# Kernel tuning notes

Hardware: AMD Instinct MI355X
Metric: run time of the kernel (lower is better)

## Reference

```python
import jax, jax.numpy as jnp
import numpy as np

EPS = 1e-5

def _layernorm(x, g, b):
    mu = jnp.mean(x, axis=-1, keepdims=True)
    var = jnp.var(x, axis=-1, keepdims=True)
    return (x - mu) * jax.lax.rsqrt(var + EPS) * g + b

def _pos_encoding(S, D, dtype):
    pos = jnp.arange(S, dtype=jnp.float32)[:, None]
    div = jnp.exp(jnp.arange(0, D, 2, dtype=jnp.float32) * (-jnp.log(10000.0) / D))
    pe = jnp.zeros((S, D), dtype=jnp.float32)
    pe = pe.at[:, 0::2].set(jnp.sin(pos * div))
    pe = pe.at[:, 1::2].set(jnp.cos(pos * div))
    return pe.astype(dtype)

def setup_inputs() -> dict:
    key = jax.random.key(0)
    B, S, D, H, F, L = 4, 1024, 768, 12, 3072, 6
    ks = jax.random.split(key, 8)
    s = 0.02
    return {
        "x": jax.random.normal(ks[0], (B, S, D), jnp.float32),
        "Wqkv": jax.random.normal(ks[1], (L, D, 3 * D), jnp.float32) * s,
        "bqkv": jnp.zeros((L, 3 * D), jnp.float32),
        "Wo": jax.random.normal(ks[2], (L, D, D), jnp.float32) * s,
        "bo": jnp.zeros((L, D), jnp.float32),
        "ln1_g": jnp.ones((L, D), jnp.float32),
        "ln1_b": jnp.zeros((L, D), jnp.float32),
        "W1": jax.random.normal(ks[3], (L, D, F), jnp.float32) * s,
        "b1": jnp.zeros((L, F), jnp.float32),
        "W2": jax.random.normal(ks[4], (L, F, D), jnp.float32) * s,
        "b2": jnp.zeros((L, D), jnp.float32),
        "ln2_g": jnp.ones((L, D), jnp.float32),
        "ln2_b": jnp.zeros((L, D), jnp.float32),
        "lnf_g": jnp.ones((D,), jnp.float32),
        "lnf_b": jnp.zeros((D,), jnp.float32),
        "num_heads": 12,
    }

def reference(x, Wqkv, bqkv, Wo, bo, ln1_g, ln1_b, W1, b1, W2, b2, ln2_g, ln2_b, lnf_g, lnf_b, num_heads):
    B, S, D = x.shape
    H = num_heads
    hd = D // H
    scale = 1.0 / jnp.sqrt(jnp.float32(hd)).astype(x.dtype)

    x = x + _pos_encoding(S, D, x.dtype)[None]

    def layer(h, params):
        wqkv, bq, wo, bo_, g1, b1_, w1, bias1, w2, bias2, g2, b2_ = params
        qkv = (h @ wqkv + bq).reshape(B, S, 3, H, hd)
        q, k, v = jnp.moveaxis(qkv, 2, 0)          # each [B,S,H,hd]
        q = q.transpose(0, 2, 1, 3)                 # bhqd
        k = k.transpose(0, 2, 1, 3)
        v = v.transpose(0, 2, 1, 3)
        scores = jnp.einsum('bhqd,bhkd->bhqk', q, k) * scale
        w = jax.nn.softmax(scores, axis=-1)
        w = jnp.clip(w, 1e-6, 1.0)                  # clamp as in torch module
        attn = jnp.einsum('bhqk,bhkd->bhqd', w, v)
        attn = attn.transpose(0, 2, 1, 3).reshape(B, S, D) @ wo + bo_
        h = _layernorm(h + attn, g1, b1_)
        ffn = jax.nn.relu(h @ w1 + bias1) @ w2 + bias2
        h = _layernorm(h + ffn, g2, b2_)
        return h, None

    params = (Wqkv, bqkv, Wo, bo, ln1_g, ln1_b, W1, b1, W2, b2, ln2_g, ln2_b)
    x, _ = jax.lax.scan(layer, x, params)
    return _layernorm(x, lnf_g, lnf_b)
```

## Files before the change

kernel.cpp:

```cpp
#include <hip/hip_runtime.h>
#include <math.h>

typedef float f32x4 __attribute__((ext_vector_type(4)));
typedef __bf16 bf16x8 __attribute__((ext_vector_type(8)));
typedef unsigned short u16x8 __attribute__((ext_vector_type(8)));

__device__ __forceinline__ unsigned short f2bf(float f) {
    union { float f; unsigned int u; } v; v.f = f;
    unsigned int r = v.u + 0x7FFFu + ((v.u >> 16) & 1u);
    return (unsigned short)(r >> 16);
}
__device__ __forceinline__ unsigned short f2bft(float f) {
    union { float f; unsigned int u; } v; v.f = f;
    return (unsigned short)(v.u >> 16);
}
__device__ __forceinline__ float bf2f(unsigned short u) {
    union { unsigned int u; float f; } v; v.u = ((unsigned int)u) << 16;
    return v.f;
}
__device__ __forceinline__ bf16x8 ld8(const unsigned short* p) {
    union { u16x8 u; bf16x8 b; } c;
    c.u = *(const u16x8*)p;
    return c.b;
}
__device__ __forceinline__ void gload_lds16(const unsigned short* g, unsigned short* l) {
    __builtin_amdgcn_global_load_lds(
        (const __attribute__((address_space(1))) unsigned int*)g,
        (__attribute__((address_space(3))) unsigned int*)l,
        16, 0, 0);
}
__device__ __forceinline__ int swz_off(int row, int quad) {
    return row * 32 + ((quad ^ ((row >> 1) & 3)) << 3);
}

__global__ __launch_bounds__(256)
void wprep_k(const float* __restrict__ Wqkv, const float* __restrict__ Wo,
             const float* __restrict__ W1, const float* __restrict__ W2,
             unsigned short* __restrict__ qkvT, unsigned short* __restrict__ woT,
             unsigned short* __restrict__ w1T, unsigned short* __restrict__ w2T) {
    __shared__ float tile[32][33];
    int bid = blockIdx.x;
    size_t ly = blockIdx.y;
    const float* W; unsigned short* Wt; int K, N, idx;
    if (bid < 1728)      { W = Wqkv + ly * 768 * 2304; Wt = qkvT + ly * 768 * 2304; K = 768;  N = 2304; idx = bid; }
    else if (bid < 2304) { W = Wo   + ly * 768 * 768;  Wt = woT  + ly * 768 * 768;  K = 768;  N = 768;  idx = bid - 1728; }
    else if (bid < 4608) { W = W1   + ly * 768 * 3072; Wt = w1T  + ly * 768 * 3072; K = 768;  N = 3072; idx = bid - 2304; }
    else                 { W = W2   + ly * 3072 * 768; Wt = w2T  + ly * 3072 * 768; K = 3072; N = 768;  idx = bid - 4608; }
    int ntile = N / 32;
    int n0 = (idx % ntile) * 32, k0 = (idx / ntile) * 32;
    int tx = threadIdx.x & 31, ty = threadIdx.x >> 5;
#pragma unroll
    for (int i = 0; i < 4; ++i) {
        int k = ty + i * 8;
        tile[k][tx] = W[(size_t)(k0 + k) * N + n0 + tx];
    }
    __syncthreads();
#pragma unroll
    for (int i = 0; i < 4; ++i) {
        int n = ty + i * 8;
        Wt[(size_t)(n0 + n) * K + k0 + tx] = f2bf(tile[tx][n]);
    }
}

__global__ __launch_bounds__(256)
void posenc_k(const float* __restrict__ x, float* __restrict__ h,
              unsigned short* __restrict__ hb) {
    int idx = blockIdx.x * 256 + threadIdx.x;
    const int TOT = 4 * 1024 * 768;
    if (idx >= TOT) return;
    int d = idx % 768;
    int s = (idx / 768) % 1024;
    int i2 = d >> 1;
    float dv = expf(-(float)(2 * i2) * (9.210340371976184f / 768.0f));
    float ang = (float)s * dv;
    float pe = (d & 1) ? cosf(ang) : sinf(ang);
    float v = x[idx] + pe;
    h[idx] = v;
    hb[idx] = f2bf(v);
}

template<int RELU, int BIAS, int QSCALE>
__global__ __launch_bounds__(256)
void gemm_k(const unsigned short* __restrict__ A, const unsigned short* __restrict__ Bt,
            const float* __restrict__ bias, unsigned short* __restrict__ Cb,
            int M, int N, int K, int Kc) {
    __shared__ unsigned short As[2][128 * 32];
    __shared__ unsigned short Bs[2][128 * 32];
    const int tid = threadIdx.x;
    const int lane = tid & 63, wave = tid >> 6;
    const int l15 = lane & 15, quad = lane >> 4;
    const int m0 = blockIdx.y * 128, n0 = blockIdx.x * 128;
    const int wr = (wave >> 1) * 64, wc = (wave & 1) * 64;
    const int kstart = blockIdx.z * Kc;
    unsigned short* Cbp = Cb + (size_t)blockIdx.z * M * N;

    const int r0 = wave * 32 + (lane >> 2);
    const int kc0 = lane & 3;

    auto stage = [&](int k0, int bi) {
#pragma unroll
        for (int j = 0; j < 2; ++j) {
            int r = r0 + j * 16;
            int kcl = kc0 ^ ((r >> 1) & 3);
            gload_lds16(A + (size_t)(m0 + r) * K + k0 + kcl * 8,
                        &As[bi][(wave * 32 + j * 16) * 32]);
            gload_lds16(Bt + (size_t)(n0 + r) * K + k0 + kcl * 8,
                        &Bs[bi][(wave * 32 + j * 16) * 32]);
        }
    };

    f32x4 acc[4][4];
#pragma unroll
    for (int i = 0; i < 4; ++i)
#pragma unroll
        for (int j = 0; j < 4; ++j) acc[i][j] = (f32x4){0.f, 0.f, 0.f, 0.f};

    stage(kstart, 0);
    const int nk = Kc / 32;
    for (int t = 0; t < nk; ++t) {
        __syncthreads();
        if (t + 1 < nk) stage(kstart + (t + 1) * 32, (t + 1) & 1);
        const unsigned short* Asb = As[t & 1];
        const unsigned short* Bsb = Bs[t & 1];
        bf16x8 af[4], bfr[4];
#pragma unroll
        for (int mt = 0; mt < 4; ++mt)
            af[mt] = ld8(&Asb[swz_off(wr + mt * 16 + l15, quad)]);
#pragma unroll
        for (int nt = 0; nt < 4; ++nt)
            bfr[nt] = ld8(&Bsb[swz_off(wc + nt * 16 + l15, quad)]);
#pragma unroll
        for (int mt = 0; mt < 4; ++mt)
#pragma unroll
            for (int nt = 0; nt < 4; ++nt)
                acc[mt][nt] = __builtin_amdgcn_mfma_f32_16x16x32_bf16(
                    af[mt], bfr[nt], acc[mt][nt], 0, 0, 0);
    }
    const float scl = (QSCALE && n0 < 768) ? 0.18033688088889765f : 1.0f;
#pragma unroll
    for (int mt = 0; mt < 4; ++mt)
#pragma unroll
        for (int nt = 0; nt < 4; ++nt)
#pragma unroll
            for (int r = 0; r < 4; ++r) {
                int row = m0 + wr + mt * 16 + quad * 4 + r;
                int col = n0 + wc + nt * 16 + l15;
                float v = acc[mt][nt][r];
                if (BIAS) v += bias[col];
                if (QSCALE) v *= scl;
                if (RELU) v = fmaxf(v, 0.f);
                Cbp[(size_t)row * N + col] = f2bf(v);
            }
}

__global__ __launch_bounds__(256)
void vt_prep(const unsigned short* __restrict__ qkv, unsigned short* __restrict__ Vt) {
    __shared__ unsigned short t[64][65];
    int bh = blockIdx.y, s0 = blockIdx.x * 64;
    int b = bh / 12, h = bh % 12;
    int tid = threadIdx.x;
    int tx = tid & 63, ty = tid >> 6;
#pragma unroll
    for (int r = 0; r < 16; ++r) {
        int i = ty + r * 4;
        t[i][tx] = qkv[(size_t)(b * 1024 + s0 + i) * 2304 + 1536 + h * 64 + tx];
    }
    __syncthreads();
#pragma unroll
    for (int r = 0; r < 16; ++r) {
        int dd = ty + r * 4;
        Vt[((size_t)bh * 64 + dd) * 1024 + s0 + tx] = t[tx][dd];
    }
}

__global__ __launch_bounds__(256)
void flash_k(const unsigned short* __restrict__ QKV, const unsigned short* __restrict__ Vt,
             unsigned short* __restrict__ O2, float* __restrict__ ls) {
    const int S = 1024, HD = 64;
    int bh = blockIdx.y, b = bh / 12, h = bh % 12;
    int q0 = blockIdx.x * 64;
    int zz = blockIdx.z;
    const unsigned short* Qp = QKV + (size_t)(b * 1024 + q0) * 2304 + h * 64;
    const unsigned short* Kp = QKV + (size_t)(b * 1024) * 2304 + 768 + h * 64;
    const unsigned short* Vp = Vt + (size_t)bh * HD * S;

    __shared__ unsigned short sm[20480];
    unsigned short* Qs = sm;

    int tid = threadIdx.x, lane = tid & 63, wave = tid >> 6;
    int l15 = lane & 15, quad = lane >> 4;
    const int rl0 = lane >> 2, c0 = lane & 3;

#pragma unroll
    for (int j = 0; j < 2; ++j) {
        int R = wave * 32 + j * 16 + rl0;
        int khalf = R >> 6, grow = R & 63;
        int lch = c0 ^ ((R >> 1) & 3);
        gload_lds16(Qp + (size_t)grow * 2304 + khalf * 32 + lch * 8,
                    &Qs[(wave * 32 + j * 16) * 32]);
    }
    __syncthreads();
    bf16x8 qa0 = ld8(&Qs[swz_off(wave * 16 + l15, quad)]);
    bf16x8 qa1 = ld8(&Qs[swz_off(64 + wave * 16 + l15, quad)]);

    auto stageKV = [&](int kt, int bi) {
        unsigned short* Ksb = sm + 4096 + bi * 4096;
        unsigned short* Vsb = sm + 12288 + bi * 4096;
#pragma unroll
        for (int j = 0; j < 2; ++j) {
            int R = wave * 32 + j * 16 + rl0;
            int khalf = R >> 6, grow = R & 63;
            int lch = c0 ^ ((R >> 1) & 3);
            gload_lds16(Kp + (size_t)(kt * 64 + grow) * 2304 + khalf * 32 + lch * 8,
                        &Ksb[(wave * 32 + j * 16) * 32]);
            gload_lds16(Vp + (size_t)grow * S + kt * 64 + khalf * 32 + lch * 8,
                        &Vsb[(wave * 32 + j * 16) * 32]);
        }
    };

    f32x4 o[4];
#pragma unroll
    for (int i = 0; i < 4; ++i) o[i] = (f32x4){0.f, 0.f, 0.f, 0.f};
    f32x4 lacc = (f32x4){0.f, 0.f, 0.f, 0.f};
    bf16x8 ones;
    {
        union { u16x8 u; bf16x8 b; } c;
#pragma unroll
        for (int j = 0; j < 8; ++j) c.u[j] = 0x3F80;
        ones = c.b;
    }
    unsigned short* Pw = sm + wave * 1024;

    stageKV(zz * 8, 0);
    for (int i = 0; i < 8; ++i) {
        int kt = zz * 8 + i;
        __syncthreads();
        if (i < 7) stageKV(kt + 1, (i + 1) & 1);
        const unsigned short* Ks = sm + 4096 + (i & 1) * 4096;
        const unsigned short* Vs = sm + 12288 + (i & 1) * 4096;

        f32x4 sc[4];
#pragma unroll
        for (int cb = 0; cb < 4; ++cb) {
            bf16x8 kb0 = ld8(&Ks[swz_off(cb * 16 + l15, quad)]);
            bf16x8 kb1 = ld8(&Ks[swz_off(64 + cb * 16 + l15, quad)]);
            f32x4 z = (f32x4){0.f, 0.f, 0.f, 0.f};
            z = __builtin_amdgcn_mfma_f32_16x16x32_bf16(qa0, kb0, z, 0, 0, 0);
            z = __builtin_amdgcn_mfma_f32_16x16x32_bf16(qa1, kb1, z, 0, 0, 0);
            sc[cb] = z;
        }
#pragma unroll
        for (int cb = 0; cb < 4; ++cb)
#pragma unroll
            for (int r = 0; r < 4; ++r)
                Pw[(quad * 4 + r) * 64 + ((cb * 16 + l15) ^ (quad << 4))] =
                    f2bft(__builtin_amdgcn_exp2f(sc[cb][r]));
        bf16x8 pa0 = ld8(&Pw[l15 * 64 + ((quad * 8) ^ ((l15 >> 2) << 4))]);
        bf16x8 pa1 = ld8(&Pw[l15 * 64 + ((32 + quad * 8) ^ ((l15 >> 2) << 4))]);
        lacc = __builtin_amdgcn_mfma_f32_16x16x32_bf16(pa0, ones, lacc, 0, 0, 0);
        lacc = __builtin_amdgcn_mfma_f32_16x16x32_bf16(pa1, ones, lacc, 0, 0, 0);
#pragma unroll
        for (int cb = 0; cb < 4; ++cb) {
            bf16x8 vb0 = ld8(&Vs[swz_off(cb * 16 + l15, quad)]);
            bf16x8 vb1 = ld8(&Vs[swz_off(64 + cb * 16 + l15, quad)]);
            o[cb] = __builtin_amdgcn_mfma_f32_16x16x32_bf16(pa0, vb0, o[cb], 0, 0, 0);
            o[cb] = __builtin_amdgcn_mfma_f32_16x16x32_bf16(pa1, vb1, o[cb], 0, 0, 0);
        }
    }
    unsigned short* Op = O2 + (size_t)zz * 4096 * 768;
#pragma unroll
    for (int cb = 0; cb < 4; ++cb)
#pragma unroll
        for (int r = 0; r < 4; ++r) {
            int row = q0 + wave * 16 + quad * 4 + r;
            Op[((size_t)(b * 1024 + row)) * 768 + h * 64 + cb * 16 + l15] =
                f2bf(o[cb][r]);
        }
    if (l15 == 0) {
#pragma unroll
        for (int r = 0; r < 4; ++r)
            ls[zz * 49152 + bh * 1024 + q0 + wave * 16 + quad * 4 + r] = lacc[r];
    }
}

__global__ __launch_bounds__(256)
void attn_combine_k(const unsigned short* __restrict__ O2, const float* __restrict__ ls,
                    unsigned short* __restrict__ ctx) {
    int idx = blockIdx.x * 256 + threadIdx.x;
    int ch = idx % 96;
    int row = idx / 96;
    int col = ch * 8;
    int b = row >> 10, s = row & 1023, h = col >> 6;
    const size_t MD = (size_t)4096 * 768;
    u16x8 o0 = *(const u16x8*)&O2[(size_t)row * 768 + col];
    u16x8 o1 = *(const u16x8*)&O2[MD + (size_t)row * 768 + col];
    int li = (b * 12 + h) * 1024 + s;
    float rl = 1.0f / (ls[li] + ls[49152 + li]);
    u16x8 ov;
#pragma unroll
    for (int j = 0; j < 8; ++j)
        ov[j] = f2bf((bf2f(o0[j]) + bf2f(o1[j])) * rl);
    *(u16x8*)&ctx[(size_t)row * 768 + col] = ov;
}

template<int NPART, int WBF16>
__global__ __launch_bounds__(256)
void ln_k(const float* __restrict__ X, const unsigned short* __restrict__ P,
          const float* __restrict__ pb,
          const float* __restrict__ g, const float* __restrict__ bta,
          float* __restrict__ Yf, unsigned short* __restrict__ Yb) {
    const int D = 768;
    const size_t MD = (size_t)4096 * 768;
    int row = blockIdx.x;
    int tid = threadIdx.x;
    const float* x = X + (size_t)row * D;
    float v[3];
    float s = 0.f, s2 = 0.f;
#pragma unroll
    for (int i = 0; i < 3; ++i) {
        int c = i * 256 + tid;
        float t = x[c];
        if (NPART > 0) {
            float r = pb[c];
#pragma unroll
            for (int pi = 0; pi < NPART; ++pi)
                r += bf2f(P[MD * pi + (size_t)row * D + c]);
            t += r;
        }
        v[i] = t;
        s += t;
        s2 += t * t;
    }
#pragma unroll
    for (int off = 1; off < 64; off <<= 1) {
        s += __shfl_xor(s, off);
        s2 += __shfl_xor(s2, off);
    }
    __shared__ float rs[4], rs2[4];
    int wave = tid >> 6, lane = tid & 63;
    if (lane == 0) { rs[wave] = s; rs2[wave] = s2; }
    __syncthreads();
    s = rs[0] + rs[1] + rs[2] + rs[3];
    s2 = rs2[0] + rs2[1] + rs2[2] + rs2[3];
    float mu = s * (1.f / 768.f);
    float var = s2 * (1.f / 768.f) - mu * mu;
    float rstd = rsqrtf(var + 1e-5f);
#pragma unroll
    for (int i = 0; i < 3; ++i) {
        int c = i * 256 + tid;
        float y = (v[i] - mu) * rstd * g[c] + bta[c];
        Yf[(size_t)row * D + c] = y;
        if (WBF16) Yb[(size_t)row * D + c] = f2bf(y);
    }
}

extern "C" void kernel_launch(void* const* d_in, const int* in_sizes, int n_in,
                              void* d_out, int out_size, void* d_ws, size_t ws_size,
                              hipStream_t stream) {
    const float* x    = (const float*)d_in[0];
    const float* Wqkv = (const float*)d_in[1];
    const float* bqkv = (const float*)d_in[2];
    const float* Wo   = (const float*)d_in[3];
    const float* bo   = (const float*)d_in[4];
    const float* ln1g = (const float*)d_in[5];
    const float* ln1b = (const float*)d_in[6];
    const float* W1   = (const float*)d_in[7];
    const float* b1   = (const float*)d_in[8];
    const float* W2   = (const float*)d_in[9];
    const float* b2   = (const float*)d_in[10];
    const float* ln2g = (const float*)d_in[11];
    const float* ln2b = (const float*)d_in[12];
    const float* lnfg = (const float*)d_in[13];
    const float* lnfb = (const float*)d_in[14];

    const int B = 4, S = 1024, D = 768, H = 12, F = 3072, L = 6;
    const int M = B * S;

    const int WL = (ws_size >= (size_t)200 * 1024 * 1024) ? 6 : 1;

    char* p = (char*)d_ws;
    auto alloc = [&](size_t bytes) -> char* {
        char* r = p;
        p += (bytes + 255) & ~(size_t)255;
        return r;
    };
    float* h             = (float*)alloc((size_t)M * D * 4);
    unsigned short* tmp  = (unsigned short*)alloc((size_t)4 * M * D * 2);
    float* lsbuf         = (float*)alloc((size_t)2 * 48 * 1024 * 4);
    unsigned short* hb   = (unsigned short*)alloc((size_t)M * D * 2);
    unsigned short* act  = (unsigned short*)alloc((size_t)M * F * 2);
    unsigned short* Vtb  = (unsigned short*)alloc((size_t)M * D * 2);
    unsigned short* ctx  = (unsigned short*)alloc((size_t)M * D * 2);
    unsigned short* wqkvT = (unsigned short*)alloc((size_t)WL * 3 * D * D * 2);
    unsigned short* woT   = (unsigned short*)alloc((size_t)WL * D * D * 2);
    unsigned short* w1T   = (unsigned short*)alloc((size_t)WL * D * F * 2);
    unsigned short* w2T   = (unsigned short*)alloc((size_t)WL * D * F * 2);
    unsigned short* qkvb = act;
    unsigned short* f1b  = act;

    posenc_k<<<(M * D) / 256, 256, 0, stream>>>(x, h, hb);
    if (WL == 6)
        wprep_k<<<dim3(6912, 6), 256, 0, stream>>>(Wqkv, Wo, W1, W2,
                                                   wqkvT, woT, w1T, w2T);

    for (int l = 0; l < L; ++l) {
        if (WL == 1)
            wprep_k<<<dim3(6912, 1), 256, 0, stream>>>(
                Wqkv + (size_t)l * D * 3 * D, Wo + (size_t)l * D * D,
                W1 + (size_t)l * D * F, W2 + (size_t)l * F * D,
                wqkvT, woT, w1T, w2T);
        size_t lo = (WL == 6) ? (size_t)l : 0;
        const unsigned short* qT  = wqkvT + lo * 3 * D * D;
        const unsigned short* oT  = woT   + lo * D * D;
        const unsigned short* f1T = w1T   + lo * D * F;
        const unsigned short* f2T = w2T   + lo * D * F;

        gemm_k<0, 1, 1><<<dim3(3 * D / 128, M / 128, 1), 256, 0, stream>>>(
            hb, qT, bqkv + (size_t)l * 3 * D, qkvb, M, 3 * D, D, D);
        vt_prep<<<dim3(S / 64, B * H), 256, 0, stream>>>(qkvb, Vtb);
        flash_k<<<dim3(S / 64, B * H, 2), 256, 0, stream>>>(qkvb, Vtb, tmp, lsbuf);
        attn_combine_k<<<(M * 96) / 256, 256, 0, stream>>>(tmp, lsbuf, ctx);
        gemm_k<0, 0, 0><<<dim3(D / 128, M / 128, 4), 256, 0, stream>>>(
            ctx, oT, nullptr, tmp, M, D, D, D / 4);
        ln_k<4, 1><<<M, 256, 0, stream>>>(h, tmp, bo + (size_t)l * D,
                                          ln1g + (size_t)l * D, ln1b + (size_t)l * D,
                                          h, hb);
        gemm_k<1, 1, 0><<<dim3(F / 128, M / 128, 1), 256, 0, stream>>>(
            hb, f1T, b1 + (size_t)l * F, f1b, M, F, D, D);
        gemm_k<0, 0, 0><<<dim3(D / 128, M / 128, 4), 256, 0, stream>>>(
            f1b, f2T, nullptr, tmp, M, D, F, F / 4);
        ln_k<4, 1><<<M, 256, 0, stream>>>(h, tmp, b2 + (size_t)l * D,
                                          ln2g + (size_t)l * D, ln2b + (size_t)l * D,
                                          h, hb);
    }
    ln_k<0, 0><<<M, 256, 0, stream>>>(h, nullptr, nullptr, lnfg, lnfb,
                                      (float*)d_out, nullptr);
}
```

Measured before the change: 1.185 ms.

## Drop flash split-K and combine kernel; halve GEMM split-K partitions

The attention kernel now walks all 16 key tiles in one block instead of splitting them across two z-slices. It normalizes the output by the row sum in-register and writes ctx directly, which removes the attn_combine kernel and its partial-output and row-sum round trip. The Wo and W2 GEMMs now use 2 split-K partitions instead of 4, and the layernorm kernels read 2 partials instead of 4. The price is half as many attention blocks (768) and fewer GEMM blocks, so parallelism drops on a large GPU.

```diff
diff --git a/kernel.cpp b/kernel.cpp
--- a/kernel.cpp
+++ b/kernel.cpp
@@ -175,11 +175,10 @@
 
 __global__ __launch_bounds__(256)
 void flash_k(const unsigned short* __restrict__ QKV, const unsigned short* __restrict__ Vt,
-             unsigned short* __restrict__ O2, float* __restrict__ ls) {
+             unsigned short* __restrict__ ctx) {
     const int S = 1024, HD = 64;
     int bh = blockIdx.y, b = bh / 12, h = bh % 12;
     int q0 = blockIdx.x * 64;
-    int zz = blockIdx.z;
     const unsigned short* Qp = QKV + (size_t)(b * 1024 + q0) * 2304 + h * 64;
     const unsigned short* Kp = QKV + (size_t)(b * 1024) * 2304 + 768 + h * 64;
     const unsigned short* Vp = Vt + (size_t)bh * HD * S;
@@ -231,11 +230,10 @@
     }
     unsigned short* Pw = sm + wave * 1024;
 
-    stageKV(zz * 8, 0);
-    for (int i = 0; i < 8; ++i) {
-        int kt = zz * 8 + i;
+    stageKV(0, 0);
+    for (int i = 0; i < 16; ++i) {
         __syncthreads();
-        if (i < 7) stageKV(kt + 1, (i + 1) & 1);
+        if (i < 15) stageKV(i + 1, (i + 1) & 1);
         const unsigned short* Ks = sm + 4096 + (i & 1) * 4096;
         const unsigned short* Vs = sm + 12288 + (i & 1) * 4096;
 
@@ -267,40 +265,17 @@
             o[cb] = __builtin_amdgcn_mfma_f32_16x16x32_bf16(pa1, vb1, o[cb], 0, 0, 0);
         }
     }
-    unsigned short* Op = O2 + (size_t)zz * 4096 * 768;
+    float inv[4];
+#pragma unroll
+    for (int r = 0; r < 4; ++r) inv[r] = 1.0f / lacc[r];
 #pragma unroll
     for (int cb = 0; cb < 4; ++cb)
 #pragma unroll
         for (int r = 0; r < 4; ++r) {
             int row = q0 + wave * 16 + quad * 4 + r;
-            Op[((size_t)(b * 1024 + row)) * 768 + h * 64 + cb * 16 + l15] =
-                f2bf(o[cb][r]);
-        }
-    if (l15 == 0) {
-#pragma unroll
-        for (int r = 0; r < 4; ++r)
-            ls[zz * 49152 + bh * 1024 + q0 + wave * 16 + quad * 4 + r] = lacc[r];
-    }
-}
-
-__global__ __launch_bounds__(256)
-void attn_combine_k(const unsigned short* __restrict__ O2, const float* __restrict__ ls,
-                    unsigned short* __restrict__ ctx) {
-    int idx = blockIdx.x * 256 + threadIdx.x;
-    int ch = idx % 96;
-    int row = idx / 96;
-    int col = ch * 8;
-    int b = row >> 10, s = row & 1023, h = col >> 6;
-    const size_t MD = (size_t)4096 * 768;
-    u16x8 o0 = *(const u16x8*)&O2[(size_t)row * 768 + col];
-    u16x8 o1 = *(const u16x8*)&O2[MD + (size_t)row * 768 + col];
-    int li = (b * 12 + h) * 1024 + s;
-    float rl = 1.0f / (ls[li] + ls[49152 + li]);
-    u16x8 ov;
-#pragma unroll
-    for (int j = 0; j < 8; ++j)
-        ov[j] = f2bf((bf2f(o0[j]) + bf2f(o1[j])) * rl);
-    *(u16x8*)&ctx[(size_t)row * 768 + col] = ov;
+            ctx[((size_t)(b * 1024 + row)) * 768 + h * 64 + cb * 16 + l15] =
+                f2bf(o[cb][r] * inv[r]);
+        }
 }
 
 template<int NPART, int WBF16>
@@ -385,8 +360,7 @@
         return r;
     };
     float* h             = (float*)alloc((size_t)M * D * 4);
-    unsigned short* tmp  = (unsigned short*)alloc((size_t)4 * M * D * 2);
-    float* lsbuf         = (float*)alloc((size_t)2 * 48 * 1024 * 4);
+    unsigned short* tmp  = (unsigned short*)alloc((size_t)2 * M * D * 2);
     unsigned short* hb   = (unsigned short*)alloc((size_t)M * D * 2);
     unsigned short* act  = (unsigned short*)alloc((size_t)M * F * 2);
     unsigned short* Vtb  = (unsigned short*)alloc((size_t)M * D * 2);
@@ -418,18 +392,17 @@
         gemm_k<0, 1, 1><<<dim3(3 * D / 128, M / 128, 1), 256, 0, stream>>>(
             hb, qT, bqkv + (size_t)l * 3 * D, qkvb, M, 3 * D, D, D);
         vt_prep<<<dim3(S / 64, B * H), 256, 0, stream>>>(qkvb, Vtb);
-        flash_k<<<dim3(S / 64, B * H, 2), 256, 0, stream>>>(qkvb, Vtb, tmp, lsbuf);
-        attn_combine_k<<<(M * 96) / 256, 256, 0, stream>>>(tmp, lsbuf, ctx);
-        gemm_k<0, 0, 0><<<dim3(D / 128, M / 128, 4), 256, 0, stream>>>(
-            ctx, oT, nullptr, tmp, M, D, D, D / 4);
-        ln_k<4, 1><<<M, 256, 0, stream>>>(h, tmp, bo + (size_t)l * D,
+        flash_k<<<dim3(S / 64, B * H), 256, 0, stream>>>(qkvb, Vtb, ctx);
+        gemm_k<0, 0, 0><<<dim3(D / 128, M / 128, 2), 256, 0, stream>>>(
+            ctx, oT, nullptr, tmp, M, D, D, D / 2);
+        ln_k<2, 1><<<M, 256, 0, stream>>>(h, tmp, bo + (size_t)l * D,
                                           ln1g + (size_t)l * D, ln1b + (size_t)l * D,
                                           h, hb);
         gemm_k<1, 1, 0><<<dim3(F / 128, M / 128, 1), 256, 0, stream>>>(
             hb, f1T, b1 + (size_t)l * F, f1b, M, F, D, D);
-        gemm_k<0, 0, 0><<<dim3(D / 128, M / 128, 4), 256, 0, stream>>>(
-            f1b, f2T, nullptr, tmp, M, D, F, F / 4);
-        ln_k<4, 1><<<M, 256, 0, stream>>>(h, tmp, b2 + (size_t)l * D,
+        gemm_k<0, 0, 0><<<dim3(D / 128, M / 128, 2), 256, 0, stream>>>(
+            f1b, f2T, nullptr, tmp, M, D, F, F / 2);
+        ln_k<2, 1><<<M, 256, 0, stream>>>(h, tmp, b2 + (size_t)l * D,
                                           ln2g + (size_t)l * D, ln2b + (size_t)l * D,
                                           h, hb);
     }
```

New measurement: 1.172 ms. No clear change (-1.1%).
